# Optimization experiments

Hardware: AMD Instinct MI355X
Metric: run time of the kernel (lower is better)

The kernel has to match this reference:

```python
import jax, jax.numpy as jnp
import numpy as np

N_NODES = 100000
N_EDGES = 1600000
N_CLUSTERS = 1024
EPS = 1e-5


def gcn_conv(x, W, b, src, dst, n, ew=None):
    """PyG GCNConv: symmetric norm with self-loops. ew: optional edge weight/mask."""
    h = x @ W
    if ew is None:
        ew = jnp.ones(src.shape[0], h.dtype)
    deg = jax.ops.segment_sum(ew, dst, num_segments=n) + 1.0  # +1 self loop
    dinv = jax.lax.rsqrt(deg)
    coef = dinv[src] * dinv[dst] * ew  # [E]
    out = jax.ops.segment_sum(h[src] * coef[:, None], dst, num_segments=n)
    out = out + h * (dinv * dinv)[:, None]  # self-loop messages
    return out + b


def instance_norm(x):
    # PyG InstanceNorm, batch=None -> single graph, no affine, biased variance
    mu = jnp.mean(x, axis=0, keepdims=True)
    var = jnp.mean((x - mu) ** 2, axis=0, keepdims=True)
    return (x - mu) * jax.lax.rsqrt(var + EPS)


def forward(x, WG1, bG1, WfG1, bfG1, WG2, bG2, WfG2, bfG2,
            WL1, bL1, WfL1, bfL1, WL2, bL2, WfL2, bfL2,
            WO1, bO1, WfO1, bfO1, WO2, bO2, WfO2, bfO2, WO3, bO3, WfO3, bfO3,
            adj, in_batch, cluster):
    elu = jax.nn.elu
    n = x.shape[0]
    src, dst = adj[0], adj[1]
    # global GCN stack
    h = elu(gcn_conv(x, WG1, bG1, src, dst, n))
    h = elu(h @ WfG1 + bfG1)
    h = elu(gcn_conv(h, WG2, bG2, src, dst, n))
    h = elu(h @ WfG2 + bfG2)
    y = instance_norm(h)  # [N, 256]
    # avg_pool over clusters (single graph -> batch offset is 0 but kept faithful)
    bc = cluster + in_batch * N_CLUSTERS  # [N]
    cnt = jax.ops.segment_sum(jnp.ones(n, y.dtype), bc, num_segments=N_CLUSTERS)
    px = jax.ops.segment_sum(y, bc, num_segments=N_CLUSTERS) / jnp.maximum(cnt, 1.0)[:, None]
    # pool edges: map through cluster, remove self-loops, coalesce (dedupe via sort+mask)
    psrc, pdst = bc[src], bc[dst]
    key = psrc * N_CLUSTERS + pdst
    order = jnp.argsort(key)
    ks = key[order]
    s2, d2 = psrc[order], pdst[order]
    first = jnp.concatenate([jnp.ones((1,), bool), ks[1:] != ks[:-1]])
    emask = (first & (s2 != d2)).astype(y.dtype)
    # local GCN stack on compressed graph
    lx = elu(gcn_conv(px, WL1, bL1, s2, d2, N_CLUSTERS, emask))
    lx = elu(lx @ WfL1 + bfL1)
    lx = elu(gcn_conv(lx, WL2, bL2, s2, d2, N_CLUSTERS, emask))
    lx = elu(lx @ WfL2 + bfL2)  # [C, 64]
    # gather-broadcast compressed features back to nodes
    comp = lx[bc]  # [N, 64]
    z = jnp.concatenate([y, comp], axis=1)  # [N, 320]
    z = elu(gcn_conv(z, WO1, bO1, src, dst, n))
    z = elu(z @ WfO1 + bfO1)
    z = elu(gcn_conv(z, WO2, bO2, src, dst, n))
    z = elu(z @ WfO2 + bfO2)
    z = elu(gcn_conv(z, WO3, bO3, src, dst, n))
    z = elu(z @ WfO3 + bfO3)
    return z


def _lin(key, i, o):
    k1, k2 = jax.random.split(key)
    s = 1.0 / np.sqrt(i)
    return (jax.random.normal(k1, (i, o), jnp.float32) * s,
            jax.random.normal(k2, (o,), jnp.float32) * s)


def setup_inputs() -> dict:
    key = jax.random.key(0)
    ks = jax.random.split(key, 20)
    inp = {}
    inp['x'] = jax.random.normal(ks[0], (N_NODES, 3), jnp.float32)
    inp['adj'] = jax.random.randint(ks[1], (2, N_EDGES), 0, N_NODES, jnp.int64 if jax.config.jax_enable_x64 else jnp.int32)
    inp['num_graphs'] = 1
    inp['in_batch'] = jnp.zeros((N_NODES,), jnp.int32)
    inp['cluster'] = jax.random.randint(ks[2], (N_NODES,), 0, N_CLUSTERS, jnp.int32)
    dims = [('G1', 3, 64), ('fG1', 64, 64), ('G2', 64, 256), ('fG2', 256, 256),
            ('L1', 256, 128), ('fL1', 128, 128), ('L2', 128, 64), ('fL2', 64, 64),
            ('O1', 320, 128), ('fO1', 128, 128), ('O2', 128, 32), ('fO2', 32, 32),
            ('O3', 32, 3), ('fO3', 3, 3)]
    for j, (name, i, o) in enumerate(dims):
        W, b = _lin(ks[3 + j], i, o)
        inp['W' + name] = W
        inp['b' + name] = b
    return inp


def reference(x, adj, num_graphs, in_batch, cluster,
              WG1, bG1, WfG1, bfG1, WG2, bG2, WfG2, bfG2,
              WL1, bL1, WfL1, bfL1, WL2, bL2, WfL2, bfL2,
              WO1, bO1, WfO1, bfO1, WO2, bO2, WfO2, bfO2, WO3, bO3, WfO3, bfO3):
    return forward(x, WG1, bG1, WfG1, bfG1, WG2, bG2, WfG2, bfG2,
                   WL1, bL1, WfL1, bfL1, WL2, bL2, WfL2, bfL2,
                   WO1, bO1, WfO1, bfO1, WO2, bO2, WfO2, bfO2,
                   WO3, bO3, WfO3, bfO3, adj, in_batch, cluster)
```

## Files before the change

kernel.cpp:

```cpp
#include <hip/hip_runtime.h>


#define NCLUST 1024

typedef short bf16x8 __attribute__((ext_vector_type(8)));
typedef float f32x4 __attribute__((ext_vector_type(4)));

__device__ __forceinline__ float elu1(float x) { return x > 0.f ? x : expm1f(x); }

__device__ __forceinline__ unsigned f2bf(float f) {
    union { float f; unsigned u; } c; c.f = f;
    unsigned u = c.u;
    return (u + 0x7fffu + ((u >> 16) & 1u)) >> 16;
}
__device__ __forceinline__ float bf2f(unsigned h) {
    union { unsigned u; float f; } c; c.u = h << 16; return c.f;
}

union U8 { unsigned u[4]; bf16x8 v; };

__device__ __forceinline__ void wpack_body(const float* W, unsigned* Phi, unsigned* Plo,
                                           int K, int BN, int t) {
    int NT = BN / 16;
    int lane = t & 63;
    int rest = t >> 6;
    int ct = rest % NT;
    int s = rest / NT;
    int col = ct * 16 + (lane & 15);
    int g = lane >> 4;
    int k0 = s * 32;
    float e[8];
#pragma unroll
    for (int j = 0; j < 4; j++) {
        e[j]     = W[(size_t)(k0 + 4 * g + j) * BN + col];
        e[4 + j] = W[(size_t)(k0 + 16 + 4 * g + j) * BN + col];
    }
#pragma unroll
    for (int j = 0; j < 4; j++) {
        unsigned h0 = f2bf(e[2 * j]), h1 = f2bf(e[2 * j + 1]);
        Phi[(size_t)t * 4 + j] = h0 | (h1 << 16);
        unsigned l0 = f2bf(e[2 * j] - bf2f(h0));
        unsigned l1 = f2bf(e[2 * j + 1] - bf2f(h1));
        Plo[(size_t)t * 4 + j] = l0 | (l1 << 16);
    }
}

struct PackDesc { const float* W; unsigned* Ph; unsigned* Pl; int K, BN, tbase; };
struct InitArgs {
    PackDesc d[6]; int tot;
    int4* z1; int nz1; int4* z2; int nz2;
};

__global__ void k_init(InitArgs a) {
    int t = blockIdx.x * 256 + threadIdx.x;
    if (t < a.nz1) a.z1[t] = make_int4(0, 0, 0, 0);
    else if (t - a.nz1 < a.nz2) a.z2[t - a.nz1] = make_int4(0, 0, 0, 0);
    if (t < a.tot) {
        int i = 0;
#pragma unroll
        for (int j = 1; j < 6; j++) if (t >= a.d[j].tbase) i = j;
        wpack_body(a.d[i].W, a.d[i].Ph, a.d[i].Pl, a.d[i].K, a.d[i].BN,
                   t - a.d[i].tbase);
    }
}

__global__ void k_hist(const int* __restrict__ key, int* __restrict__ deg, int E) {
    int e = blockIdx.x * 256 + threadIdx.x;
    if (e < E) atomicAdd(&deg[key[e]], 1);
}

__global__ void k_scan_block(const int* __restrict__ deg, int* __restrict__ rowptr,
                             int* __restrict__ bsum, int n) {
    __shared__ int lds[256];
    int tid = threadIdx.x;
    int base = blockIdx.x * 1024 + tid * 4;
    int v0 = base + 0 < n ? deg[base + 0] : 0;
    int v1 = base + 1 < n ? deg[base + 1] : 0;
    int v2 = base + 2 < n ? deg[base + 2] : 0;
    int v3 = base + 3 < n ? deg[base + 3] : 0;
    int tsum = v0 + v1 + v2 + v3;
    lds[tid] = tsum; __syncthreads();
    for (int off = 1; off < 256; off <<= 1) {
        int t = (tid >= off) ? lds[tid - off] : 0;
        __syncthreads();
        lds[tid] += t;
        __syncthreads();
    }
    int run = lds[tid] - tsum;
    if (base + 0 < n) rowptr[base + 0] = run; run += v0;
    if (base + 1 < n) rowptr[base + 1] = run; run += v1;
    if (base + 2 < n) rowptr[base + 2] = run; run += v2;
    if (base + 3 < n) rowptr[base + 3] = run;
    if (tid == 255) bsum[blockIdx.x] = lds[255];
}

__global__ void k_nodeinit(int* __restrict__ rowptr, const int* __restrict__ bsum,
                           const int* __restrict__ deg, const int* __restrict__ cluster,
                           const int* __restrict__ inb, float* __restrict__ dinv,
                           int* __restrict__ bc, int* __restrict__ cdeg, int n, int nb) {
    __shared__ int pfx[128];
    int tid = threadIdx.x;
    if (tid < 128) pfx[tid] = (tid < nb) ? bsum[tid] : 0;
    __syncthreads();
    for (int off = 1; off < 128; off <<= 1) {
        int v = 0;
        if (tid < 128 && tid >= off) v = pfx[tid - off];
        __syncthreads();
        if (tid < 128) pfx[tid] += v;
        __syncthreads();
    }
    int i = blockIdx.x * 256 + tid;
    if (i >= n) return;
    int j = i >> 10;
    int base = (j == 0) ? 0 : pfx[j - 1];
    rowptr[i] += base;
    dinv[i] = rsqrtf((float)deg[i] + 1.0f);
    int c = cluster[i] + inb[i] * NCLUST;
    bc[i] = c;
    atomicAdd(&cdeg[c], 1);
}

__global__ void k_fillc(const int* __restrict__ src, const int* __restrict__ dst,
                        const float* __restrict__ dinv, const int* __restrict__ rowptr,
                        int* __restrict__ fill, int2* __restrict__ csr_ev, int E,
                        const int* __restrict__ bc, const int* __restrict__ crowptr,
                        int* __restrict__ cfill, int* __restrict__ cnodes, int n) {
    int e = blockIdx.x * 256 + threadIdx.x;
    if (e < E) {
        int d = dst[e];
        int pos = rowptr[d] + atomicAdd(&fill[d], 1);
        int s = src[e];
        csr_ev[pos] = make_int2(s, __float_as_int(dinv[s]));
    }
    if (e < n) {
        int c = bc[e];
        int pos = crowptr[c] + atomicAdd(&cfill[c], 1);
        cnodes[pos] = e;
    }
}

template <int F, int OB>
__global__ __launch_bounds__(256) void k_prop4sb(
        const unsigned short* __restrict__ hbf, const float* __restrict__ dinv,
        const int* __restrict__ rowptr, const int* __restrict__ deg,
        const int2* __restrict__ csr_ev,
        const float* __restrict__ bias, float* __restrict__ outf,
        unsigned short* __restrict__ outb, int n, int flags) {
    constexpr int FS = F / 4;
    constexpr int ES = 64 / FS;
    const int node = (blockIdx.x * 256 + threadIdx.x) >> 6;
    if (node >= n) return;
    const int l = threadIdx.x & 63;
    const int fs = l & (FS - 1);
    const int ep = l / FS;
    const int fi = fs * 4;
    const int start = rowptr[node];
    const int cnt = deg[node];
    float ax = 0.f, ay = 0.f, az = 0.f, aw = 0.f;
    for (int j = ep; j < cnt; j += ES) {
        const int2 ev = csr_ev[start + j];
        int s = ev.x;
        float w = __int_as_float(ev.y);
        const ushort4 v = *reinterpret_cast<const ushort4*>(&hbf[(size_t)s * F + fi]);
        ax += w * bf2f(v.x); ay += w * bf2f(v.y);
        az += w * bf2f(v.z); aw += w * bf2f(v.w);
    }
#pragma unroll
    for (int off = FS; off < 64; off <<= 1) {
        ax += __shfl_xor(ax, off);
        ay += __shfl_xor(ay, off);
        az += __shfl_xor(az, off);
        aw += __shfl_xor(aw, off);
    }
    if (ep == 0) {
        float di = dinv[node];
        const ushort4 sv = *reinterpret_cast<const ushort4*>(&hbf[(size_t)node * F + fi]);
        float4 o;
        o.x = di * ax + di * di * bf2f(sv.x);
        o.y = di * ay + di * di * bf2f(sv.y);
        o.z = di * az + di * di * bf2f(sv.z);
        o.w = di * aw + di * di * bf2f(sv.w);
        if (flags) {
            const float4 b = *reinterpret_cast<const float4*>(&bias[fi]);
            o.x = elu1(o.x + b.x); o.y = elu1(o.y + b.y);
            o.z = elu1(o.z + b.z); o.w = elu1(o.w + b.w);
        }
        if constexpr (OB) {
            ushort4 ob;
            ob.x = (unsigned short)f2bf(o.x); ob.y = (unsigned short)f2bf(o.y);
            ob.z = (unsigned short)f2bf(o.z); ob.w = (unsigned short)f2bf(o.w);
            *reinterpret_cast<ushort4*>(&outb[(size_t)node * F + fi]) = ob;
        } else {
            *reinterpret_cast<float4*>(&outf[(size_t)node * F + fi]) = o;
        }
    }
}

__global__ void k_prop3f1(const float* __restrict__ h, const float* __restrict__ dinv,
                          const int* __restrict__ rowptr, const int* __restrict__ deg,
                          const int2* __restrict__ csr_ev,
                          const float* __restrict__ WG1, const float* __restrict__ bG1,
                          unsigned short* __restrict__ outb, int n) {
    int node = blockIdx.x * 256 + threadIdx.x;
    if (node >= n) return;
    int start = rowptr[node], cnt = deg[node];
    float a0 = 0.f, a1 = 0.f, a2 = 0.f;
    for (int j = 0; j < cnt; j++) {
        const int2 ev = csr_ev[start + j];
        int s = ev.x;
        float w = __int_as_float(ev.y);
        a0 += w * h[(size_t)s * 3 + 0];
        a1 += w * h[(size_t)s * 3 + 1];
        a2 += w * h[(size_t)s * 3 + 2];
    }
    float di = dinv[node];
    float p0 = di * a0 + di * di * h[(size_t)node * 3 + 0];
    float p1 = di * a1 + di * di * h[(size_t)node * 3 + 1];
    float p2 = di * a2 + di * di * h[(size_t)node * 3 + 2];
    unsigned short* op = outb + (size_t)node * 64;
#pragma unroll 4
    for (int c = 0; c < 64; c += 4) {
        ushort4 ob;
        ob.x = (unsigned short)f2bf(elu1(p0 * WG1[c + 0] + p1 * WG1[64 + c + 0] + p2 * WG1[128 + c + 0] + bG1[c + 0]));
        ob.y = (unsigned short)f2bf(elu1(p0 * WG1[c + 1] + p1 * WG1[64 + c + 1] + p2 * WG1[128 + c + 1] + bG1[c + 1]));
        ob.z = (unsigned short)f2bf(elu1(p0 * WG1[c + 2] + p1 * WG1[64 + c + 2] + p2 * WG1[128 + c + 2] + bG1[c + 2]));
        ob.w = (unsigned short)f2bf(elu1(p0 * WG1[c + 3] + p1 * WG1[64 + c + 3] + p2 * WG1[128 + c + 3] + bG1[c + 3]));
        *reinterpret_cast<ushort4*>(op + c) = ob;
    }
}

__global__ void k_prop3out(const float* __restrict__ h, const float* __restrict__ dinv,
                           const int* __restrict__ rowptr, const int* __restrict__ deg,
                           const int2* __restrict__ csr_ev,
                           const float* __restrict__ bO3, const float* __restrict__ WfO3,
                           const float* __restrict__ bfO3, float* __restrict__ out, int n) {
    int node = blockIdx.x * 256 + threadIdx.x;
    if (node >= n) return;
    int start = rowptr[node], cnt = deg[node];
    float a0 = 0.f, a1 = 0.f, a2 = 0.f;
    for (int j = 0; j < cnt; j++) {
        const int2 ev = csr_ev[start + j];
        int s = ev.x;
        float w = __int_as_float(ev.y);
        a0 += w * h[(size_t)s * 3 + 0];
        a1 += w * h[(size_t)s * 3 + 1];
        a2 += w * h[(size_t)s * 3 + 2];
    }
    float di = dinv[node];
    float o0 = elu1(di * a0 + di * di * h[(size_t)node * 3 + 0] + bO3[0]);
    float o1 = elu1(di * a1 + di * di * h[(size_t)node * 3 + 1] + bO3[1]);
    float o2 = elu1(di * a2 + di * di * h[(size_t)node * 3 + 2] + bO3[2]);
#pragma unroll
    for (int c = 0; c < 3; c++) {
        out[(size_t)node * 3 + c] =
            elu1(o0 * WfO3[c] + o1 * WfO3[3 + c] + o2 * WfO3[6 + c] + bfO3[c]);
    }
}

__global__ void k_normprep(const float* __restrict__ W, const float* __restrict__ insum,
                           const float* __restrict__ insumsq, unsigned* __restrict__ Phi,
                           unsigned* __restrict__ Plo, float* __restrict__ corr,
                           float* __restrict__ mu, float* __restrict__ rstd, int n) {
    const float fn = (float)n;
    const int bid = blockIdx.x, tid = threadIdx.x;
    if (bid == 16) {
        float m = insum[tid] / fn;
        float var = insumsq[tid] / fn - m * m;
        mu[tid] = m;
        rstd[tid] = rsqrtf(var + 1e-5f);
        return;
    }
    {
        int t = bid * 256 + tid;
        int lane = t & 63, rest = t >> 6;
        int ct = rest % 8, s = rest / 8;
        int col = ct * 16 + (lane & 15);
        int g = lane >> 4;
        int k0 = s * 32;
        float e[8];
#pragma unroll
        for (int j = 0; j < 4; j++) {
            int ka = k0 + 4 * g + j;
            int kb = k0 + 16 + 4 * g + j;
            float ma = insum[ka] / fn;
            float sa = rsqrtf(insumsq[ka] / fn - ma * ma + 1e-5f);
            float mb = insum[kb] / fn;
            float sb = rsqrtf(insumsq[kb] / fn - mb * mb + 1e-5f);
            e[j]     = W[(size_t)ka * 128 + col] * sa;
            e[4 + j] = W[(size_t)kb * 128 + col] * sb;
        }
#pragma unroll
        for (int j = 0; j < 4; j++) {
            unsigned h0 = f2bf(e[2 * j]), h1 = f2bf(e[2 * j + 1]);
            Phi[(size_t)t * 4 + j] = h0 | (h1 << 16);
            unsigned l0 = f2bf(e[2 * j] - bf2f(h0));
            unsigned l1 = f2bf(e[2 * j + 1] - bf2f(h1));
            Plo[(size_t)t * 4 + j] = l0 | (l1 << 16);
        }
    }
    if (tid < 128) {
        int k0 = bid * 16;
        float s = 0.f;
        for (int k = k0; k < k0 + 16; k++) {
            float m = insum[k] / fn;
            float r = rsqrtf(insumsq[k] / fn - m * m + 1e-5f);
            s += m * r * W[(size_t)k * 128 + tid];
        }
        atomicAdd(&corr[tid], s);
    }
}

template <int BN, int WAVES, int FULLW>
__global__ __launch_bounds__(WAVES * 64) void k_gmfma(
        const unsigned short* __restrict__ Abf,
        const unsigned* __restrict__ Phi, const unsigned* __restrict__ Plo,
        const float* __restrict__ bias, const float* __restrict__ sub,
        const float* __restrict__ add, const int* __restrict__ addidx,
        float* __restrict__ C, unsigned short* __restrict__ Cbf,
        const float* __restrict__ W3, float* __restrict__ C3,
        int N, int K, int flags) {
    constexpr int NT = BN / 16;
    constexpr int WCOL = (BN == 256) ? 4 : (BN == 128 ? 2 : 1);
    constexpr int WROW = WAVES / WCOL;
    constexpr int NTW = NT / WCOL;
    constexpr int BR = 32 * WROW;
    constexpr bool LDSW = (BN >= 128);
    constexpr int LDSU = (FULLW > 0) ? 2 * NT * (FULLW / 32) * 256
                                     : (LDSW ? 2 * 2 * NT * 256 : 1);
    __shared__ unsigned lds_w[LDSU];
    const int t = threadIdx.x;
    const int w = t >> 6, l = t & 63;
    const int wr = w / WCOL, wc = w % WCOL;
    const int l15 = l & 15, g = l >> 4;
    const int row0 = blockIdx.x * BR + wr * 32;
    const int ctbase = wc * NTW;
    int ar0 = row0 + l15;      ar0 = ar0 < N ? ar0 : N - 1;
    int ar1 = row0 + 16 + l15; ar1 = ar1 < N ? ar1 : N - 1;
    const unsigned short* ab0 = Abf + (size_t)ar0 * K;
    const unsigned short* ab1 = Abf + (size_t)ar1 * K;

    f32x4 acc[2][NTW];
#pragma unroll
    for (int f = 0; f < 2; f++)
#pragma unroll
        for (int ct = 0; ct < NTW; ct++) acc[f][ct] = (f32x4){0.f, 0.f, 0.f, 0.f};

    auto loadA = [&](int s, U8* ahi) {
        const int k0 = s * 32;
#pragma unroll
        for (int f = 0; f < 2; f++) {
            const unsigned short* ab = f ? ab1 : ab0;
            const uint2 hA = *reinterpret_cast<const uint2*>(ab + k0 + 4 * g);
            const uint2 hB = *reinterpret_cast<const uint2*>(ab + k0 + 16 + 4 * g);
            ahi[f].u[0] = hA.x; ahi[f].u[1] = hA.y;
            ahi[f].u[2] = hB.x; ahi[f].u[3] = hB.y;
        }
    };
    auto domfma = [&](U8* wh, U8* wl, U8* ahi) {
#pragma unroll
        for (int ct = 0; ct < NTW; ct++) {
            acc[0][ct] = __builtin_amdgcn_mfma_f32_16x16x32_bf16(ahi[0].v, wh[ct].v, acc[0][ct], 0, 0, 0);
            acc[0][ct] = __builtin_amdgcn_mfma_f32_16x16x32_bf16(ahi[0].v, wl[ct].v, acc[0][ct], 0, 0, 0);
            acc[1][ct] = __builtin_amdgcn_mfma_f32_16x16x32_bf16(ahi[1].v, wh[ct].v, acc[1][ct], 0, 0, 0);
            acc[1][ct] = __builtin_amdgcn_mfma_f32_16x16x32_bf16(ahi[1].v, wl[ct].v, acc[1][ct], 0, 0, 0);
        }
    };

    const int nk = K / 32;

    if constexpr (FULLW > 0) {
        constexpr int NKT = FULLW / 32;
        for (int i = w; i < 2 * NT * NKT; i += WAVES) {
            int s = i / (2 * NT);
            int j = i - s * 2 * NT;
            const unsigned* gsrc = (j < NT)
                ? Phi + (size_t)(s * NT + j) * 256 + l * 4
                : Plo + (size_t)(s * NT + (j - NT)) * 256 + l * 4;
            __builtin_amdgcn_global_load_lds(
                (const __attribute__((address_space(1))) unsigned*)gsrc,
                (__attribute__((address_space(3))) unsigned*)(lds_w + (size_t)i * 256),
                16, 0, 0);
        }
        __syncthreads();
        U8 wh[NTW], wl[NTW], ahiA[2];
#pragma unroll
        for (int s = 0; s < NKT; s++) {
            loadA(s, ahiA);
            const unsigned* base = lds_w + (size_t)s * (2 * NT * 256);
#pragma unroll
            for (int ct = 0; ct < NTW; ct++) {
                wh[ct] = *reinterpret_cast<const U8*>(base + (ctbase + ct) * 256 + l * 4);
                wl[ct] = *reinterpret_cast<const U8*>(base + (NT + ctbase + ct) * 256 + l * 4);
            }
            domfma(wh, wl, ahiA);
        }
        __syncthreads();
    } else if constexpr (LDSW) {
        auto stage = [&](int s, int b) {
            unsigned* base = lds_w + (size_t)b * (2 * NT * 256);
            for (int i = w; i < 2 * NT; i += WAVES) {
                const unsigned* gsrc = (i < NT)
                    ? Phi + (size_t)(s * NT + i) * 256 + l * 4
                    : Plo + (size_t)(s * NT + (i - NT)) * 256 + l * 4;
                __builtin_amdgcn_global_load_lds(
                    (const __attribute__((address_space(1))) unsigned*)gsrc,
                    (__attribute__((address_space(3))) unsigned*)(base + i * 256),
                    16, 0, 0);
            }
        };
        auto loadWlds = [&](int b, U8* wh, U8* wl) {
            const unsigned* base = lds_w + (size_t)b * (2 * NT * 256);
#pragma unroll
            for (int ct = 0; ct < NTW; ct++) {
                wh[ct] = *reinterpret_cast<const U8*>(base + (ctbase + ct) * 256 + l * 4);
                wl[ct] = *reinterpret_cast<const U8*>(base + (NT + ctbase + ct) * 256 + l * 4);
            }
        };

        U8 wh[NTW], wl[NTW], ahiA[2], ahiB[2];
        stage(0, 0);
        loadA(0, ahiA);
        __syncthreads();
        int s = 0;
        while (true) {
            const bool hasB = (s + 1 < nk);
            if (hasB) { stage(s + 1, (s + 1) & 1); loadA(s + 1, ahiB); }
            loadWlds(s & 1, wh, wl);
            domfma(wh, wl, ahiA);
            __syncthreads();
            if (!hasB) break;
            s++;
            const bool hasA2 = (s + 1 < nk);
            if (hasA2) { stage(s + 1, (s + 1) & 1); loadA(s + 1, ahiA); }
            loadWlds(s & 1, wh, wl);
            domfma(wh, wl, ahiB);
            __syncthreads();
            if (!hasA2) break;
            s++;
        }
    } else {
        auto loadW = [&](int s, U8* wh, U8* wl) {
            const unsigned* pb = Phi + ((size_t)(s * NT + ctbase) * 64 + l) * 4;
            const unsigned* pl = Plo + ((size_t)(s * NT + ctbase) * 64 + l) * 4;
#pragma unroll
            for (int ct = 0; ct < NTW; ct++) {
                wh[ct] = *reinterpret_cast<const U8*>(pb + (size_t)ct * 256);
                wl[ct] = *reinterpret_cast<const U8*>(pl + (size_t)ct * 256);
            }
        };
        U8 whA[NTW], wlA[NTW], ahiA[2];
        U8 whB[NTW], wlB[NTW], ahiB[2];
        loadW(0, whA, wlA);
        loadA(0, ahiA);
        int s = 0;
        while (true) {
            const bool hasB = (s + 1 < nk);
            if (hasB) { loadW(s + 1, whB, wlB); loadA(s + 1, ahiB); }
            domfma(whA, wlA, ahiA);
            if (!hasB) break;
            const bool hasA2 = (s + 2 < nk);
            if (hasA2) { loadW(s + 2, whA, wlA); loadA(s + 2, ahiA); }
            domfma(whB, wlB, ahiB);
            if (!hasA2) break;
            s += 2;
        }
        __syncthreads();
    }

#pragma unroll
    for (int f = 0; f < 2; f++) {
#pragma unroll
        for (int r = 0; r < 4; r++) {
            int row = row0 + 16 * f + 4 * g + r;
            if (row >= N) continue;
            int gi = (add != nullptr) ? addidx[row] : 0;
            float t0 = 0.f, t1 = 0.f, t2 = 0.f;
#pragma unroll
            for (int ct = 0; ct < NTW; ct++) {
                int col = (ctbase + ct) * 16 + l15;
                float o = acc[f][ct][r];
                if (add != nullptr) o += add[(size_t)gi * BN + col];
                if (sub != nullptr) o -= sub[col];
                if (flags) o = elu1(o + bias[col]);
                if (C != nullptr) C[(size_t)row * BN + col] = o;
                if (Cbf != nullptr) Cbf[(size_t)row * BN + col] = (unsigned short)f2bf(o);
                if (W3 != nullptr) {
                    t0 += o * W3[col * 3 + 0];
                    t1 += o * W3[col * 3 + 1];
                    t2 += o * W3[col * 3 + 2];
                }
            }
            if (W3 != nullptr) {
#pragma unroll
                for (int m = 1; m < 16; m <<= 1) {
                    t0 += __shfl_xor(t0, m);
                    t1 += __shfl_xor(t1, m);
                    t2 += __shfl_xor(t2, m);
                }
                if (l15 == 0) {
                    C3[(size_t)row * 3 + 0] = t0;
                    C3[(size_t)row * 3 + 1] = t1;
                    C3[(size_t)row * 3 + 2] = t2;
                }
            }
        }
    }
}

template <int M, int RPT>
__global__ __launch_bounds__(256) void k_fc(
        const float* __restrict__ A, const float* __restrict__ W,
        const float* __restrict__ bias, const float* __restrict__ add,
        const int* __restrict__ addidx, float* __restrict__ C,
        int N, int K, int flags) {
    constexpr int TX = M / 4;
    constexpr int TY = 256 / TX;
    constexpr int RB = TY * RPT;
    int tx = threadIdx.x % TX;
    int ty = threadIdx.x / TX;
    int row0 = blockIdx.x * RB + ty * RPT;
    float4 acc[RPT];
#pragma unroll
    for (int r = 0; r < RPT; r++) acc[r] = make_float4(0.f, 0.f, 0.f, 0.f);
    for (int k = 0; k < K; k++) {
        float4 w = *reinterpret_cast<const float4*>(&W[(size_t)k * M + tx * 4]);
#pragma unroll
        for (int r = 0; r < RPT; r++) {
            int row = row0 + r;
            row = row < N ? row : N - 1;
            float a = A[(size_t)row * K + k];
            acc[r].x += a * w.x; acc[r].y += a * w.y;
            acc[r].z += a * w.z; acc[r].w += a * w.w;
        }
    }
    if (add != nullptr) {
#pragma unroll
        for (int r = 0; r < RPT; r++) {
            int row = row0 + r;
            if (row < N) {
                int g = addidx[row];
                const float4 v = *reinterpret_cast<const float4*>(&add[(size_t)g * M + tx * 4]);
                acc[r].x += v.x; acc[r].y += v.y; acc[r].z += v.z; acc[r].w += v.w;
            }
        }
    }
    __syncthreads();
    float4 b = make_float4(0.f, 0.f, 0.f, 0.f);
    if (flags) b = *reinterpret_cast<const float4*>(&bias[tx * 4]);
#pragma unroll
    for (int r = 0; r < RPT; r++) {
        int row = row0 + r;
        if (row >= N) break;
        float4 o = acc[r];
        o.x += b.x; o.y += b.y; o.z += b.z; o.w += b.w;
        if (flags) { o.x = elu1(o.x); o.y = elu1(o.y); o.z = elu1(o.z); o.w = elu1(o.w); }
        *reinterpret_cast<float4*>(&C[(size_t)row * M + tx * 4]) = o;
    }
}

__global__ __launch_bounds__(256) void k_fcl2(
        const float* __restrict__ A, const float* __restrict__ W1,
        const float* __restrict__ b1, const float* __restrict__ W2,
        float* __restrict__ lxout, float* __restrict__ compO) {
    __shared__ float lx[32][64];
    const int tid = threadIdx.x;
    const int tx = tid % 16, ty = tid / 16;
    const int row0b = blockIdx.x * 32;
    float4 acc[2];
    acc[0] = make_float4(0.f, 0.f, 0.f, 0.f);
    acc[1] = make_float4(0.f, 0.f, 0.f, 0.f);
    for (int k = 0; k < 64; k++) {
        float4 w = *reinterpret_cast<const float4*>(&W1[(size_t)k * 64 + tx * 4]);
#pragma unroll
        for (int r = 0; r < 2; r++) {
            float a = A[(size_t)(row0b + ty * 2 + r) * 64 + k];
            acc[r].x += a * w.x; acc[r].y += a * w.y;
            acc[r].z += a * w.z; acc[r].w += a * w.w;
        }
    }
    float4 b = *reinterpret_cast<const float4*>(&b1[tx * 4]);
#pragma unroll
    for (int r = 0; r < 2; r++) {
        int lr = ty * 2 + r;
        float4 o;
        o.x = elu1(acc[r].x + b.x); o.y = elu1(acc[r].y + b.y);
        o.z = elu1(acc[r].z + b.z); o.w = elu1(acc[r].w + b.w);
        *reinterpret_cast<float4*>(&lxout[(size_t)(row0b + lr) * 64 + tx * 4]) = o;
        lx[lr][tx * 4 + 0] = o.x; lx[lr][tx * 4 + 1] = o.y;
        lx[lr][tx * 4 + 2] = o.z; lx[lr][tx * 4 + 3] = o.w;
    }
    __syncthreads();
    for (int o = tid; o < 32 * 128; o += 256) {
        int r = o >> 7, c = o & 127;
        float s = 0.f;
        for (int k = 0; k < 64; k++) s += lx[r][k] * W2[(size_t)k * 128 + c];
        compO[(size_t)(row0b + r) * 128 + c] = s;
    }
}

__global__ void k_instats(const unsigned short* __restrict__ h, float* __restrict__ sum,
                          float* __restrict__ sumsq, int n) {
    int c = threadIdx.x;
    int r0 = blockIdx.x * 128;
    int r1 = r0 + 128 < n ? r0 + 128 : n;
    float s = 0.f, q = 0.f;
#pragma unroll 4
    for (int r = r0; r < r1; r++) {
        float v = bf2f(h[(size_t)r * 256 + c]);
        s += v; q += v * v;
    }
    atomicAdd(&sum[c], s);
    atomicAdd(&sumsq[c], q);
}

__global__ __launch_bounds__(256) void k_poolmerge(
        const unsigned short* __restrict__ xh, const int* __restrict__ crowptr,
        const int* __restrict__ cdeg, const int* __restrict__ cnodes,
        const float* __restrict__ mu, const float* __restrict__ rstd,
        float* __restrict__ px,
        const int* __restrict__ src, const int* __restrict__ dst,
        const int* __restrict__ bc, unsigned char* __restrict__ bmT, int E) {
    int bid = blockIdx.x;
    if (bid < NCLUST) {
        int cl = bid;
        int c  = threadIdx.x;
        int start = crowptr[cl];
        int cnt = cdeg[cl];
        float acc = 0.f;
        int j = 0;
        for (; j + 3 < cnt; j += 4) {
            int n0 = cnodes[start + j + 0];
            int n1 = cnodes[start + j + 1];
            int n2 = cnodes[start + j + 2];
            int n3 = cnodes[start + j + 3];
            float v0 = bf2f(xh[(size_t)n0 * 256 + c]);
            float v1 = bf2f(xh[(size_t)n1 * 256 + c]);
            float v2 = bf2f(xh[(size_t)n2 * 256 + c]);
            float v3 = bf2f(xh[(size_t)n3 * 256 + c]);
            acc += (v0 + v1) + (v2 + v3);
        }
        for (; j < cnt; j++) {
            int node = cnodes[start + j];
            acc += bf2f(xh[(size_t)node * 256 + c]);
        }
        float res = acc / fmaxf((float)cnt, 1.0f);
        res = (cnt > 0) ? (res - mu[c]) * rstd[c] : 0.f;
        px[(size_t)cl * 256 + c] = res;
    } else {
        int e = (bid - NCLUST) * 256 + threadIdx.x;
        if (e < E) {
            int ps = bc[src[e]];
            int pd = bc[dst[e]];
            bmT[(size_t)pd * NCLUST + ps] = 1;
        }
    }
}

__global__ __launch_bounds__(256) void k_pooldeg(
        const unsigned char* __restrict__ bmT, float* __restrict__ dinvp) {
    int d = blockIdx.x;
    int t = threadIdx.x;
    const unsigned int v = reinterpret_cast<const unsigned int*>(bmT + (size_t)d * NCLUST)[t];
    int s = (v & 0xff) + ((v >> 8) & 0xff) + ((v >> 16) & 0xff) + ((v >> 24) & 0xff);
    if (t == (d >> 2)) s -= (v >> ((d & 3) * 8)) & 0xff;
    __shared__ int red[256];
    red[t] = s; __syncthreads();
    for (int o = 128; o > 0; o >>= 1) {
        if (t < o) red[t] += red[t + o];
        __syncthreads();
    }
    if (t == 0) dinvp[d] = rsqrtf((float)red[0] + 1.0f);
}

template <int F>
__global__ __launch_bounds__(1024) void k_proppool2(
        const float* __restrict__ h, const float* __restrict__ dinvp,
        const unsigned char* __restrict__ bmT, const float* __restrict__ bias,
        float* __restrict__ out) {
    constexpr int SG = 1024 / F;
    const int d = blockIdx.x;
    const int t = threadIdx.x;
    const int f = t & (F - 1);
    const int sg = t / F;
    const unsigned char* bmrow = bmT + (size_t)d * NCLUST;
    float acc = 0.f;
#pragma unroll 4
    for (int s = sg; s < NCLUST; s += SG) {
        float m = (s != d) ? (float)bmrow[s] : 0.f;
        acc += m * dinvp[s] * h[(size_t)s * F + f];
    }
    __shared__ float red[1024];
    red[t] = acc; __syncthreads();
#pragma unroll
    for (int o = SG / 2; o > 0; o >>= 1) {
        if (sg < o) red[t] += red[t + o * F];
        __syncthreads();
    }
    if (sg == 0) {
        float di = dinvp[d];
        float r = di * red[f] + di * di * h[(size_t)d * F + f] + bias[f];
        out[(size_t)d * F + f] = elu1(r);
    }
}

extern "C" void kernel_launch(void* const* d_in, const int* in_sizes, int n_in,
                              void* d_out, int out_size, void* d_ws, size_t ws_size,
                              hipStream_t stream) {
    const float* x       = (const float*)d_in[0];
    const int*   adj     = (const int*)d_in[1];
    const int*   inb     = (const int*)d_in[3];
    const int*   cluster = (const int*)d_in[4];
    const float* WG1  = (const float*)d_in[5];   const float* bG1  = (const float*)d_in[6];
    const float* WfG1 = (const float*)d_in[7];   const float* bfG1 = (const float*)d_in[8];
    const float* WG2  = (const float*)d_in[9];   const float* bG2  = (const float*)d_in[10];
    const float* WfG2 = (const float*)d_in[11];  const float* bfG2 = (const float*)d_in[12];
    const float* WL1  = (const float*)d_in[13];  const float* bL1  = (const float*)d_in[14];
    const float* WfL1 = (const float*)d_in[15];  const float* bfL1 = (const float*)d_in[16];
    const float* WL2  = (const float*)d_in[17];  const float* bL2  = (const float*)d_in[18];
    const float* WfL2 = (const float*)d_in[19];  const float* bfL2 = (const float*)d_in[20];
    const float* WO1  = (const float*)d_in[21];  const float* bO1  = (const float*)d_in[22];
    const float* WfO1 = (const float*)d_in[23];  const float* bfO1 = (const float*)d_in[24];
    const float* WO2  = (const float*)d_in[25];  const float* bO2  = (const float*)d_in[26];
    const float* WfO2 = (const float*)d_in[27];  const float* bfO2 = (const float*)d_in[28];
    const float* WO3  = (const float*)d_in[29];  const float* bO3  = (const float*)d_in[30];
    const float* WfO3 = (const float*)d_in[31];  const float* bfO3 = (const float*)d_in[32];
    float* out = (float*)d_out;

    const int n = in_sizes[0] / 3;
    const int E = in_sizes[1] / 2;
    const int* src = adj;
    const int* dst = adj + E;

    char* ws = (char*)d_ws;
    size_t off = 0;
    auto alloc = [&](size_t bytes) -> void* {
        void* p = ws + off;
        off = (off + bytes + 255) & ~(size_t)255;
        return p;
    };
    int*   deg     = (int*)alloc((size_t)n * 4);
    int*   fill    = (int*)alloc((size_t)n * 4);
    int*   cdeg    = (int*)alloc(NCLUST * 4);
    int*   cfill   = (int*)alloc(NCLUST * 4);
    int*   rowptr  = (int*)alloc((size_t)n * 4);
    int*   crowptr = (int*)alloc(NCLUST * 4);
    int*   cnodes  = (int*)alloc((size_t)n * 4);
    int*   bcarr   = (int*)alloc((size_t)n * 4);
    float* dinv    = (float*)alloc((size_t)n * 4);
    int*   bsum    = (int*)alloc(512);
    int2*  csr_ev  = (int2*)alloc((size_t)E * 8);
    float* X       = (float*)alloc((size_t)n * 256 * 4);
    unsigned short* Xh = (unsigned short*)alloc((size_t)n * 256 * 2);
    float* B       = (float*)alloc((size_t)n * 128 * 4);
    unsigned short* Bh = (unsigned short*)alloc((size_t)n * 128 * 2);
    float* insum   = (float*)alloc(256 * 4);
    float* insumsq = (float*)alloc(256 * 4);
    float* px      = (float*)alloc((size_t)NCLUST * 256 * 4);
    unsigned char* bmT = (unsigned char*)alloc((size_t)NCLUST * NCLUST);
    float* corr    = (float*)alloc(128 * 4);
    float* mu      = (float*)alloc(256 * 4);
    float* rstd    = (float*)alloc(256 * 4);
    float* dinvp   = (float*)alloc(NCLUST * 4);
    float* lA      = (float*)alloc((size_t)NCLUST * 128 * 4);
    float* lB      = (float*)alloc((size_t)NCLUST * 128 * 4);
    unsigned* pfG1h = (unsigned*)alloc(2048 * 4);   unsigned* pfG1l = (unsigned*)alloc(2048 * 4);
    unsigned* pG2h  = (unsigned*)alloc(8192 * 4);   unsigned* pG2l  = (unsigned*)alloc(8192 * 4);
    unsigned* pfG2h = (unsigned*)alloc(32768 * 4);  unsigned* pfG2l = (unsigned*)alloc(32768 * 4);
    unsigned* pO1h  = (unsigned*)alloc(16384 * 4);  unsigned* pO1l  = (unsigned*)alloc(16384 * 4);
    unsigned* pfO1h = (unsigned*)alloc(8192 * 4);   unsigned* pfO1l = (unsigned*)alloc(8192 * 4);
    unsigned* pO2h  = (unsigned*)alloc(2048 * 4);   unsigned* pO2l  = (unsigned*)alloc(2048 * 4);
    unsigned* pfO2h = (unsigned*)alloc(512 * 4);    unsigned* pfO2l = (unsigned*)alloc(512 * 4);
    (void)ws_size; (void)n_in; (void)out_size;

    unsigned short* Bh1 = Bh;
    unsigned short* Bh2 = Bh + (size_t)n * 64;

    auto cdiv = [](int a, int b) { return (a + b - 1) / b; };
    const int EB = cdiv(E, 256);
    const int PB = cdiv(n, 4);

    int nz1 = (int)(((char*)rowptr - (char*)deg) / 16);
    int nz2 = (int)(((char*)mu - (char*)insum) / 16);
    InitArgs ia;
    ia.d[0] = {WfG1, pfG1h, pfG1l, 64, 64, 0};
    ia.d[1] = {WG2,  pG2h,  pG2l,  64, 256, 512};
    ia.d[2] = {WfG2, pfG2h, pfG2l, 256, 256, 2560};
    ia.d[3] = {WfO1, pfO1h, pfO1l, 128, 128, 10752};
    ia.d[4] = {WO2,  pO2h,  pO2l,  128, 32, 12800};
    ia.d[5] = {WfO2, pfO2h, pfO2l, 32, 32, 13312};
    ia.tot = 13440;
    ia.z1 = (int4*)deg; ia.nz1 = nz1;
    ia.z2 = (int4*)insum; ia.nz2 = nz2;
    int initN = (nz1 + nz2 > ia.tot) ? (nz1 + nz2) : ia.tot;
    k_init<<<cdiv(initN, 256), 256, 0, stream>>>(ia);

    k_hist<<<EB, 256, 0, stream>>>(dst, deg, E);
    int nb = cdiv(n, 1024);
    k_scan_block<<<nb, 256, 0, stream>>>(deg, rowptr, bsum, n);
    k_nodeinit<<<cdiv(n, 256), 256, 0, stream>>>(rowptr, bsum, deg, cluster, inb,
                                                 dinv, bcarr, cdeg, n, nb);
    k_scan_block<<<1, 256, 0, stream>>>(cdeg, crowptr, bsum, NCLUST);
    k_fillc<<<EB, 256, 0, stream>>>(src, dst, dinv, rowptr, fill, csr_ev, E,
                                    bcarr, crowptr, cfill, cnodes, n);

    k_prop3f1<<<cdiv(n, 256), 256, 0, stream>>>(x, dinv, rowptr, deg, csr_ev,
                                                WG1, bG1, Bh1, n);
    k_gmfma<64, 8, 0><<<cdiv(n, 256), 512, 0, stream>>>(Bh1, pfG1h, pfG1l, bfG1,
                                                        nullptr, nullptr, nullptr,
                                                        nullptr, Bh1, nullptr, nullptr,
                                                        n, 64, 1);
    k_prop4sb<64, 1><<<PB, 256, 0, stream>>>(Bh1, dinv, rowptr, deg, csr_ev,
                                             nullptr, nullptr, Bh2, n, 0);
    k_gmfma<256, 8, 64><<<cdiv(n, 64), 512, 0, stream>>>(Bh2, pG2h, pG2l, bG2,
                                                         nullptr, nullptr, nullptr,
                                                         nullptr, Xh, nullptr, nullptr,
                                                         n, 64, 1);
    k_gmfma<256, 8, 0><<<cdiv(n, 64), 512, 0, stream>>>(Xh, pfG2h, pfG2l, bfG2,
                                                        nullptr, nullptr, nullptr,
                                                        nullptr, Xh, nullptr, nullptr,
                                                        n, 256, 1);

    k_instats<<<cdiv(n, 128), 256, 0, stream>>>(Xh, insum, insumsq, n);
    k_normprep<<<17, 256, 0, stream>>>(WO1, insum, insumsq, pO1h, pO1l, corr, mu, rstd, n);

    k_poolmerge<<<NCLUST + EB, 256, 0, stream>>>(Xh, crowptr, cdeg, cnodes, mu, rstd, px,
                                                 src, dst, bcarr, bmT, E);
    k_pooldeg<<<NCLUST, 256, 0, stream>>>(bmT, dinvp);

    k_fc<128, 2><<<cdiv(NCLUST, 16), 256, 0, stream>>>(px, WL1, nullptr, nullptr, nullptr,
                                                       lA, NCLUST, 256, 0);
    k_proppool2<128><<<NCLUST, 1024, 0, stream>>>(lA, dinvp, bmT, bL1, lB);
    k_fc<128, 2><<<cdiv(NCLUST, 16), 256, 0, stream>>>(lB, WfL1, bfL1, nullptr, nullptr,
                                                       lA, NCLUST, 128, 1);
    k_fc<64, 2><<<cdiv(NCLUST, 32), 256, 0, stream>>>(lA, WL2, nullptr, nullptr, nullptr,
                                                      lB, NCLUST, 128, 0);
    k_proppool2<64><<<NCLUST, 1024, 0, stream>>>(lB, dinvp, bmT, bL2, lA);
    k_fcl2<<<NCLUST / 32, 256, 0, stream>>>(lA, WfL2, bfL2, WO1 + (size_t)256 * 128,
                                            lB, lA);

    k_gmfma<128, 8, 0><<<cdiv(n, 128), 512, 0, stream>>>(Xh, pO1h, pO1l, nullptr,
                                                         corr, lA, bcarr, nullptr, Bh,
                                                         nullptr, nullptr, n, 256, 0);
    k_prop4sb<128, 1><<<PB, 256, 0, stream>>>(Bh, dinv, rowptr, deg, csr_ev,
                                              bO1, nullptr, Xh, n, 1);
    k_gmfma<128, 8, 128><<<cdiv(n, 128), 512, 0, stream>>>(Xh, pfO1h, pfO1l, bfO1,
                                                           nullptr, nullptr, nullptr,
                                                           nullptr, Xh, nullptr, nullptr,
                                                           n, 128, 1);
    k_gmfma<32, 8, 0><<<cdiv(n, 256), 512, 0, stream>>>(Xh, pO2h, pO2l, nullptr,
                                                        nullptr, nullptr, nullptr,
                                                        nullptr, Bh, nullptr, nullptr,
                                                        n, 128, 0);
    k_prop4sb<32, 1><<<PB, 256, 0, stream>>>(Bh, dinv, rowptr, deg, csr_ev,
                                             bO2, nullptr, Xh, n, 1);
    k_gmfma<32, 8, 0><<<cdiv(n, 256), 512, 0, stream>>>(Xh, pfO2h, pfO2l, bfO2,
                                                        nullptr, nullptr, nullptr,
                                                        nullptr, nullptr, WO3, B,
                                                        n, 32, 1);
    k_prop3out<<<cdiv(n, 256), 256, 0, stream>>>(B, dinv, rowptr, deg, csr_ev,
                                                 bO3, WfO3, bfO3, out, n);
}
```

Before: 1.125 ms.

## Fuse instance-norm statistics into GEMM epilogue and chunk full-weight LDS path

New measurement: 1.134 ms. About the same (+0.8%).

```diff
diff --git a/kernel.cpp b/kernel.cpp
--- a/kernel.cpp
+++ b/kernel.cpp
@@ -318,6 +318,7 @@
         const float* __restrict__ add, const int* __restrict__ addidx,
         float* __restrict__ C, unsigned short* __restrict__ Cbf,
         const float* __restrict__ W3, float* __restrict__ C3,
+        float* __restrict__ ssum, float* __restrict__ ssumsq,
         int N, int K, int flags) {
     constexpr int NT = BN / 16;
     constexpr int WCOL = (BN == 256) ? 4 : (BN == 128 ? 2 : 1);
@@ -370,31 +371,35 @@
 
     if constexpr (FULLW > 0) {
         constexpr int NKT = FULLW / 32;
-        for (int i = w; i < 2 * NT * NKT; i += WAVES) {
-            int s = i / (2 * NT);
-            int j = i - s * 2 * NT;
-            const unsigned* gsrc = (j < NT)
-                ? Phi + (size_t)(s * NT + j) * 256 + l * 4
-                : Plo + (size_t)(s * NT + (j - NT)) * 256 + l * 4;
-            __builtin_amdgcn_global_load_lds(
-                (const __attribute__((address_space(1))) unsigned*)gsrc,
-                (__attribute__((address_space(3))) unsigned*)(lds_w + (size_t)i * 256),
-                16, 0, 0);
-        }
-        __syncthreads();
+        const int nchunk = K / FULLW;
         U8 wh[NTW], wl[NTW], ahiA[2];
-#pragma unroll
-        for (int s = 0; s < NKT; s++) {
-            loadA(s, ahiA);
-            const unsigned* base = lds_w + (size_t)s * (2 * NT * 256);
-#pragma unroll
-            for (int ct = 0; ct < NTW; ct++) {
-                wh[ct] = *reinterpret_cast<const U8*>(base + (ctbase + ct) * 256 + l * 4);
-                wl[ct] = *reinterpret_cast<const U8*>(base + (NT + ctbase + ct) * 256 + l * 4);
+        for (int c = 0; c < nchunk; c++) {
+            for (int i = w; i < 2 * NT * NKT; i += WAVES) {
+                int s = i / (2 * NT);
+                int j = i - s * 2 * NT;
+                int gs = c * NKT + s;
+                const unsigned* gsrc = (j < NT)
+                    ? Phi + (size_t)(gs * NT + j) * 256 + l * 4
+                    : Plo + (size_t)(gs * NT + (j - NT)) * 256 + l * 4;
+                __builtin_amdgcn_global_load_lds(
+                    (const __attribute__((address_space(1))) unsigned*)gsrc,
+                    (__attribute__((address_space(3))) unsigned*)(lds_w + (size_t)i * 256),
+                    16, 0, 0);
             }
-            domfma(wh, wl, ahiA);
-        }
-        __syncthreads();
+            __syncthreads();
+#pragma unroll
+            for (int s = 0; s < NKT; s++) {
+                loadA(c * NKT + s, ahiA);
+                const unsigned* base = lds_w + (size_t)s * (2 * NT * 256);
+#pragma unroll
+                for (int ct = 0; ct < NTW; ct++) {
+                    wh[ct] = *reinterpret_cast<const U8*>(base + (ctbase + ct) * 256 + l * 4);
+                    wl[ct] = *reinterpret_cast<const U8*>(base + (NT + ctbase + ct) * 256 + l * 4);
+                }
+                domfma(wh, wl, ahiA);
+            }
+            __syncthreads();
+        }
     } else if constexpr (LDSW) {
         auto stage = [&](int s, int b) {
             unsigned* base = lds_w + (size_t)b * (2 * NT * 256);
@@ -467,6 +472,11 @@
         __syncthreads();
     }
 
+    float sloc[NTW], qloc[NTW];
+    if (ssum != nullptr) {
+#pragma unroll
+        for (int ct = 0; ct < NTW; ct++) { sloc[ct] = 0.f; qloc[ct] = 0.f; }
+    }
 #pragma unroll
     for (int f = 0; f < 2; f++) {
 #pragma unroll
@@ -483,7 +493,14 @@
                 if (sub != nullptr) o -= sub[col];
                 if (flags) o = elu1(o + bias[col]);
                 if (C != nullptr) C[(size_t)row * BN + col] = o;
-                if (Cbf != nullptr) Cbf[(size_t)row * BN + col] = (unsigned short)f2bf(o);
+                if (Cbf != nullptr) {
+                    unsigned hb = f2bf(o);
+                    Cbf[(size_t)row * BN + col] = (unsigned short)hb;
+                    if (ssum != nullptr) {
+                        float ov = bf2f(hb);
+                        sloc[ct] += ov; qloc[ct] += ov * ov;
+                    }
+                }
                 if (W3 != nullptr) {
                     t0 += o * W3[col * 3 + 0];
                     t1 += o * W3[col * 3 + 1];
@@ -502,6 +519,19 @@
                     C3[(size_t)row * 3 + 1] = t1;
                     C3[(size_t)row * 3 + 2] = t2;
                 }
+            }
+        }
+    }
+    if (ssum != nullptr) {
+#pragma unroll
+        for (int ct = 0; ct < NTW; ct++) {
+            float s = sloc[ct], q = qloc[ct];
+            s += __shfl_xor(s, 16); q += __shfl_xor(q, 16);
+            s += __shfl_xor(s, 32); q += __shfl_xor(q, 32);
+            if (g == 0) {
+                int col = (ctbase + ct) * 16 + l15;
+                atomicAdd(&ssum[col], s);
+                atomicAdd(&ssumsq[col], q);
             }
         }
     }
@@ -596,21 +626,6 @@
         for (int k = 0; k < 64; k++) s += lx[r][k] * W2[(size_t)k * 128 + c];
         compO[(size_t)(row0b + r) * 128 + c] = s;
     }
-}
-
-__global__ void k_instats(const unsigned short* __restrict__ h, float* __restrict__ sum,
-                          float* __restrict__ sumsq, int n) {
-    int c = threadIdx.x;
-    int r0 = blockIdx.x * 128;
-    int r1 = r0 + 128 < n ? r0 + 128 : n;
-    float s = 0.f, q = 0.f;
-#pragma unroll 4
-    for (int r = r0; r < r1; r++) {
-        float v = bf2f(h[(size_t)r * 256 + c]);
-        s += v; q += v * v;
-    }
-    atomicAdd(&sum[c], s);
-    atomicAdd(&sumsq[c], q);
 }
 
 __global__ __launch_bounds__(256) void k_poolmerge(
@@ -808,19 +823,18 @@
     k_gmfma<64, 8, 0><<<cdiv(n, 256), 512, 0, stream>>>(Bh1, pfG1h, pfG1l, bfG1,
                                                         nullptr, nullptr, nullptr,
                                                         nullptr, Bh1, nullptr, nullptr,
-                                                        n, 64, 1);
+                                                        nullptr, nullptr, n, 64, 1);
     k_prop4sb<64, 1><<<PB, 256, 0, stream>>>(Bh1, dinv, rowptr, deg, csr_ev,
                                              nullptr, nullptr, Bh2, n, 0);
     k_gmfma<256, 8, 64><<<cdiv(n, 64), 512, 0, stream>>>(Bh2, pG2h, pG2l, bG2,
                                                          nullptr, nullptr, nullptr,
                                                          nullptr, Xh, nullptr, nullptr,
-                                                         n, 64, 1);
+                                                         nullptr, nullptr, n, 64, 1);
     k_gmfma<256, 8, 0><<<cdiv(n, 64), 512, 0, stream>>>(Xh, pfG2h, pfG2l, bfG2,
                                                         nullptr, nullptr, nullptr,
                                                         nullptr, Xh, nullptr, nullptr,
-                                                        n, 256, 1);
-
-    k_instats<<<cdiv(n, 128), 256, 0, stream>>>(Xh, insum, insumsq, n);
+                                                        insum, insumsq, n, 256, 1);
+
     k_normprep<<<17, 256, 0, stream>>>(WO1, insum, insumsq, pO1h, pO1l, corr, mu, rstd, n);
 
     k_poolmerge<<<NCLUST + EB, 256, 0, stream>>>(Xh, crowptr, cdeg, cnodes, mu, rstd, px,
@@ -838,25 +852,26 @@
     k_fcl2<<<NCLUST / 32, 256, 0, stream>>>(lA, WfL2, bfL2, WO1 + (size_t)256 * 128,
                                             lB, lA);
 
-    k_gmfma<128, 8, 0><<<cdiv(n, 128), 512, 0, stream>>>(Xh, pO1h, pO1l, nullptr,
-                                                         corr, lA, bcarr, nullptr, Bh,
-                                                         nullptr, nullptr, n, 256, 0);
+    k_gmfma<128, 8, 128><<<cdiv(n, 128), 512, 0, stream>>>(Xh, pO1h, pO1l, nullptr,
+                                                           corr, lA, bcarr, nullptr, Bh,
+                                                           nullptr, nullptr,
+                                                           nullptr, nullptr, n, 256, 0);
     k_prop4sb<128, 1><<<PB, 256, 0, stream>>>(Bh, dinv, rowptr, deg, csr_ev,
                                               bO1, nullptr, Xh, n, 1);
     k_gmfma<128, 8, 128><<<cdiv(n, 128), 512, 0, stream>>>(Xh, pfO1h, pfO1l, bfO1,
                                                            nullptr, nullptr, nullptr,
                                                            nullptr, Xh, nullptr, nullptr,
-                                                           n, 128, 1);
+                                                           nullptr, nullptr, n, 128, 1);
     k_gmfma<32, 8, 0><<<cdiv(n, 256), 512, 0, stream>>>(Xh, pO2h, pO2l, nullptr,
                                                         nullptr, nullptr, nullptr,
                                                         nullptr, Bh, nullptr, nullptr,
-                                                        n, 128, 0);
+                                                        nullptr, nullptr, n, 128, 0);
     k_prop4sb<32, 1><<<PB, 256, 0, stream>>>(Bh, dinv, rowptr, deg, csr_ev,
                                              bO2, nullptr, Xh, n, 1);
     k_gmfma<32, 8, 0><<<cdiv(n, 256), 512, 0, stream>>>(Xh, pfO2h, pfO2l, bfO2,
                                                         nullptr, nullptr, nullptr,
                                                         nullptr, nullptr, WO3, B,
-                                                        n, 32, 1);
+                                                        nullptr, nullptr, n, 32, 1);
     k_prop3out<<<cdiv(n, 256), 256, 0, stream>>>(B, dinv, rowptr, deg, csr_ev,
                                                  bO3, WfO3, bfO3, out, n);
 }
```
